# Kernel tuning notes

Hardware: AMD Instinct MI355X
Metric: run time of the kernel (lower is better)

The kernel has to match this reference:

```python
import jax, jax.numpy as jnp
import numpy as np

N = 50000        # nodes
E = 800000       # edges (avg degree 16)
D_IN = 128
HID = 128
K = 3


def cheb_edge_weights(row, col, n):
    # PyG ChebConv sym normalization with assumed lambda_max = 2.0:
    # L_hat = (2/lambda_max) * (I - D^-1/2 A D^-1/2) - I = -D^-1/2 A D^-1/2 (zero diagonal)
    mask = (row != col).astype(jnp.float32)  # remove_self_loops
    deg = jax.ops.segment_sum(mask, row, num_segments=n)
    dinv = jnp.where(deg > 0.0, jax.lax.rsqrt(jnp.maximum(deg, 1.0)), 0.0)
    return -dinv[row] * dinv[col] * mask  # [E]


def cheb_conv(x, row, col, w_edge, W, b, n):
    # Chebyshev recursion: Tx0=x, Tx1=L_hat x, Tx_k = 2 L_hat Tx_{k-1} - Tx_{k-2}
    def prop(h):  # sparse L_hat @ h via gather + segment_sum
        return jax.ops.segment_sum(w_edge[:, None] * h[col], row, num_segments=n)

    Tx0 = x
    out = Tx0 @ W[0]
    Tx1 = prop(Tx0)
    out = out + Tx1 @ W[1]
    for k in range(2, W.shape[0]):
        Tx2 = 2.0 * prop(Tx1) - Tx0
        out = out + Tx2 @ W[k]
        Tx0, Tx1 = Tx1, Tx2
    return out + b


def setup_inputs() -> dict:
    key = jax.random.key(0)
    ks = jax.random.split(key, 8)
    x = jax.random.normal(ks[0], (N, D_IN), dtype=jnp.float32)
    ei = jax.random.randint(ks[1], (2, E), 0, N, dtype=jnp.int32)
    s = 0.05
    W1 = jax.random.normal(ks[2], (K, D_IN, HID), dtype=jnp.float32) * s
    b1 = jnp.zeros((HID,), dtype=jnp.float32)
    W2 = jax.random.normal(ks[3], (K, HID, HID), dtype=jnp.float32) * s
    b2 = jnp.zeros((HID,), dtype=jnp.float32)
    W3 = jax.random.normal(ks[4], (K, HID, HID), dtype=jnp.float32) * s
    b3 = jnp.zeros((HID,), dtype=jnp.float32)
    return {"x": x, "ei": ei, "W1": W1, "b1": b1, "W2": W2, "b2": b2, "W3": W3, "b3": b3}


def reference(x, ei, W1, b1, W2, b2, W3, b3):
    row, col = ei[0], ei[1]
    w_edge = cheb_edge_weights(row, col, N)
    # layer chain: ChebConv -> ReLU -> dropout (eval mode: identity)
    h = jax.nn.relu(cheb_conv(x, row, col, w_edge, W1, b1, N))
    h = jax.nn.relu(cheb_conv(h, row, col, w_edge, W2, b2, N))
    h = jax.nn.relu(cheb_conv(h, row, col, w_edge, W3, b3, N))
    return h
```

## Files before the change

kernel.cpp:

```cpp
#include <hip/hip_runtime.h>
#include <hip/hip_bf16.h>

#define DFEAT 128

typedef _Float16 h2 __attribute__((ext_vector_type(2)));
typedef _Float16 f16x8 __attribute__((ext_vector_type(8)));
typedef float f32x4  __attribute__((ext_vector_type(4)));
typedef unsigned short u16x8 __attribute__((ext_vector_type(8)));

__device__ __forceinline__ unsigned short f16b(float f) {
    _Float16 hf = (_Float16)f;
    unsigned short b; __builtin_memcpy(&b, &hf, 2);
    return b;
}
__device__ __forceinline__ unsigned pack_f16(float lo, float hi) {
    return (unsigned)f16b(lo) | ((unsigned)f16b(hi) << 16);
}
__device__ __forceinline__ float h2f(h2 v) { float f; __builtin_memcpy(&f, &v, 4); return f; }
__device__ __forceinline__ h2 f2h(float f) { h2 v; __builtin_memcpy(&v, &f, 4); return v; }


__global__ void conv_kernel(const float2* __restrict__ x, unsigned* __restrict__ xb, int npk,
                            const float* __restrict__ W1, const float* __restrict__ W2,
                            const float* __restrict__ W3, unsigned short* __restrict__ Wt,
                            int* __restrict__ deg8, int N) {
    int id = blockIdx.x * blockDim.x + threadIdx.x;
    int gstride = gridDim.x * blockDim.x;
    for (int i = id; i < 8 * N; i += gstride) deg8[i] = 0;
    if (id < npk) {
        float2 v = x[id];
        xb[id] = pack_f16(v.x, v.y);
        return;
    }
    int id2 = id - npk;
    const int PER = 3 * DFEAT * DFEAT;
    if (id2 < 3 * PER) {
        int layer = id2 / PER;
        int rem = id2 - layer * PER;
        const float* W = (layer == 0) ? W1 : ((layer == 1) ? W2 : W3);
        int seg = rem >> 14;
        int k   = (rem >> 7) & 127;
        int nn  = rem & 127;
        float w = W[rem];
        if (seg == 0) w -= W[rem + 2 * DFEAT * DFEAT];
        else if (seg == 2) w *= 2.f;
        Wt[layer * PER + (seg << 14) + (nn << 7) + k] = f16b(w);
    }
}

__global__ void deg_kernel(const int* __restrict__ ei, int* __restrict__ deg8, int E, int N) {
    int e = blockIdx.x * blockDim.x + threadIdx.x;
    if (e < E) {
        int r = ei[e];
        int c = ei[E + e];
        if (r != c) atomicAdd(&deg8[(blockIdx.x & 7) * N + r], 1);
    }
}

__global__ __launch_bounds__(1024) void scan1_kernel(const int* __restrict__ deg8,
                                                     int* __restrict__ poff,
                                                     int* __restrict__ row_ptr,
                                                     int* __restrict__ bsum,
                                                     float* __restrict__ dinv, int n) {
    __shared__ int wsums[16];
    int t = threadIdx.x;
    int idx = blockIdx.x * 1024 + t;
    int tot = 0;
    if (idx < n) {
        int run = 0;
        #pragma unroll
        for (int p = 0; p < 8; ++p) {
            int d = deg8[p * n + idx];
            poff[p * n + idx] = run;
            run += d;
        }
        tot = run;
        dinv[idx] = (tot > 0) ? rsqrtf((float)tot) : 0.f;
    }
    int vi = tot;
    #pragma unroll
    for (int off = 1; off < 64; off <<= 1) {
        int x = __shfl_up(vi, off);
        if ((t & 63) >= off) vi += x;
    }
    if ((t & 63) == 63) wsums[t >> 6] = vi;
    __syncthreads();
    if (t < 16) {
        int s = wsums[t];
        int si = s;
        #pragma unroll
        for (int off = 1; off < 16; off <<= 1) {
            int x = __shfl_up(si, off);
            if (t >= off) si += x;
        }
        wsums[t] = si - s;
        if (t == 15) bsum[blockIdx.x] = si;
    }
    __syncthreads();
    if (idx < n) row_ptr[idx + 1] = wsums[t >> 6] + vi;
}

__global__ __launch_bounds__(1024) void scan3_kernel(int* __restrict__ row_ptr,
                                                     const int* __restrict__ bsum, int n) {
    __shared__ int soff;
    int t = threadIdx.x;
    if (t < 64) {
        int v = 0;
        for (int k = t; k < (int)blockIdx.x; k += 64) v += bsum[k];
        #pragma unroll
        for (int off = 32; off > 0; off >>= 1) v += __shfl_down(v, off);
        if (t == 0) soff = v;
    }
    __syncthreads();
    int idx = blockIdx.x * 1024 + t;
    if (idx == 0) row_ptr[0] = 0;
    if (idx < n) row_ptr[idx + 1] += soff;
}

__global__ void fill_kernel(const int* __restrict__ ei, const int* __restrict__ row_ptr,
                            int* __restrict__ poff, const float* __restrict__ dinv,
                            unsigned* __restrict__ e_cw, int E, int N) {
    int e = blockIdx.x * blockDim.x + threadIdx.x;
    if (e < E) {
        int r = ei[e];
        int c = ei[E + e];
        if (r != c) {
            int p = blockIdx.x & 7;
            int k = atomicAdd(&poff[p * N + r], 1);
            int pos = row_ptr[r] + k;
            float w = -dinv[r] * dinv[c];
            e_cw[pos] = (unsigned)c | ((unsigned)f16b(w) << 16);
        }
    }
}

__global__ __launch_bounds__(256) void prop_f16_kernel(
    const uint2* __restrict__ hin2, uint2* __restrict__ hout2,
    const int* __restrict__ row_ptr, const unsigned* __restrict__ e_cw, int n)
{
    int wv = __builtin_amdgcn_readfirstlane(threadIdx.x >> 6);
    int node = blockIdx.x * 4 + wv;
    if (node >= n) return;
    const int lane = threadIdx.x & 63;
    const int h = lane >> 5;
    const int s = lane & 31;
    int rs = row_ptr[node];
    int re = row_ptr[node + 1];

    h2 a01 = {(_Float16)0.f, (_Float16)0.f};
    h2 a23 = {(_Float16)0.f, (_Float16)0.f};

    for (int j = rs; j < re; j += 24) {
        uint2 vv[12]; unsigned ww[12];
        #pragma unroll
        for (int u = 0; u < 12; ++u) {
            int i0 = j + 2 * u;
            unsigned cw0 = (i0     < re) ? e_cw[i0]     : 0u;
            unsigned cw1 = (i0 + 1 < re) ? e_cw[i0 + 1] : 0u;
            unsigned cw = h ? cw1 : cw0;
            ww[u] = (cw & 0xffff0000u) | (cw >> 16);
            vv[u] = hin2[(size_t)(cw & 0xffffu) * 32 + s];
        }
        #pragma unroll
        for (int u = 0; u < 12; ++u) {
            h2 wp = f2h(__uint_as_float(ww[u]));
            a01 = f2h(__uint_as_float(vv[u].x)) * wp + a01;
            a23 = f2h(__uint_as_float(vv[u].y)) * wp + a23;
        }
    }
    a01 = a01 + f2h(__shfl_xor(h2f(a01), 32));
    a23 = a23 + f2h(__shfl_xor(h2f(a23), 32));

    if (h == 0) {
        uint2 o;
        o.x = __float_as_uint(h2f(a01));
        o.y = __float_as_uint(h2f(a23));
        hout2[(size_t)node * 32 + s] = o;
    }
}

#define WPAD 136
__global__ __launch_bounds__(256) void gemm3_mfma_kernel(
    const unsigned short* __restrict__ X0, const unsigned short* __restrict__ X1,
    const unsigned short* __restrict__ X2,
    const unsigned short* __restrict__ Wt, const float* __restrict__ bias,
    void* __restrict__ out, int n, int out_f16)
{
    __shared__ unsigned short Ws[DFEAT * WPAD];
    const int t    = threadIdx.x;
    const int wave = t >> 6;
    const int lane = t & 63;
    const int quad = lane >> 4;
    const int l16  = lane & 15;

    const int row_base = blockIdx.x * 128 + wave * 32;
    int r0 = row_base + l16;       if (r0 >= n) r0 = n - 1;
    int r1 = row_base + 16 + l16;  if (r1 >= n) r1 = n - 1;

    const unsigned short* Xps[3] = {X0, X1, X2};

    f32x4 acc[2][8];
    #pragma unroll
    for (int tt = 0; tt < 2; ++tt)
        #pragma unroll
        for (int c = 0; c < 8; ++c) acc[tt][c] = (f32x4){0.f, 0.f, 0.f, 0.f};

    const int srow = t >> 1;
    const int shalf = (t & 1) * 64;

    #pragma unroll
    for (int seg = 0; seg < 3; ++seg) {
        __syncthreads();
        const unsigned short* Wp = Wt + (seg << 14);
        #pragma unroll
        for (int i = 0; i < 8; ++i) {
            *(u16x8*)&Ws[srow * WPAD + shalf + i * 8] =
                *(const u16x8*)&Wp[srow * DFEAT + shalf + i * 8];
        }
        __syncthreads();
        const unsigned short* A0 = Xps[seg] + (size_t)r0 * DFEAT;
        const unsigned short* A1 = Xps[seg] + (size_t)r1 * DFEAT;
        #pragma unroll
        for (int kk = 0; kk < 4; ++kk) {
            const int ko = kk * 32 + quad * 8;
            f16x8 a0 = *(const f16x8*)(A0 + ko);
            f16x8 a1 = *(const f16x8*)(A1 + ko);
            #pragma unroll
            for (int c = 0; c < 8; ++c) {
                f16x8 b = *(const f16x8*)&Ws[(c * 16 + l16) * WPAD + ko];
                acc[0][c] = __builtin_amdgcn_mfma_f32_16x16x32_f16(a0, b, acc[0][c], 0, 0, 0);
                acc[1][c] = __builtin_amdgcn_mfma_f32_16x16x32_f16(a1, b, acc[1][c], 0, 0, 0);
            }
        }
    }

    #pragma unroll
    for (int tt = 0; tt < 2; ++tt) {
        int orow0 = blockIdx.x * 128 + wave * 32 + tt * 16 + quad * 4;
        #pragma unroll
        for (int c = 0; c < 8; ++c) {
            int col = c * 16 + l16;
            float bv = bias[col];
            #pragma unroll
            for (int r = 0; r < 4; ++r) {
                int orow = orow0 + r;
                if (orow < n) {
                    float v = fmaxf(acc[tt][c][r] + bv, 0.f);
                    if (out_f16)
                        ((unsigned short*)out)[(size_t)orow * DFEAT + col] = f16b(v);
                    else
                        ((float*)out)[(size_t)orow * DFEAT + col] = v;
                }
            }
        }
    }
}

extern "C" void kernel_launch(void* const* d_in, const int* in_sizes, int n_in,
                              void* d_out, int out_size, void* d_ws, size_t ws_size,
                              hipStream_t stream) {
    const float* x  = (const float*)d_in[0];
    const int*   ei = (const int*)d_in[1];
    const float* W1 = (const float*)d_in[2];
    const float* b1 = (const float*)d_in[3];
    const float* W2 = (const float*)d_in[4];
    const float* b2 = (const float*)d_in[5];
    const float* W3 = (const float*)d_in[6];
    const float* b3 = (const float*)d_in[7];

    const int N = in_sizes[0] / DFEAT;
    const int E = in_sizes[1] / 2;
    const int NPK = N * (DFEAT / 2);
    const int NB = (N + 1023) / 1024;

    unsigned* xb  = (unsigned*)d_ws;
    unsigned* t1b = xb  + NPK;
    unsigned* t2b = t1b + NPK;
    unsigned* ab  = t2b + NPK;
    unsigned short* wt = (unsigned short*)(ab + NPK);
    int*   deg8    = (int*)(wt + 3 * 3 * DFEAT * DFEAT);
    int*   poff    = deg8 + 8 * N;
    int*   row_ptr = poff + 8 * N;
    float* dinv    = (float*)(row_ptr + (N + 2));
    unsigned* e_cw = (unsigned*)(dinv + N);
    int*   bsum    = (int*)(e_cw + E);

    const int WELEM = 3 * DFEAT * DFEAT;
    const int CONVT = NPK + 3 * WELEM;
    conv_kernel<<<(CONVT + 255) / 256, 256, 0, stream>>>(
        (const float2*)x, xb, NPK, W1, W2, W3, wt, deg8, N);
    deg_kernel<<<(E + 255) / 256, 256, 0, stream>>>(ei, deg8, E, N);
    scan1_kernel<<<NB, 1024, 0, stream>>>(deg8, poff, row_ptr, bsum, dinv, N);
    scan3_kernel<<<NB, 1024, 0, stream>>>(row_ptr, bsum, N);
    fill_kernel<<<(E + 255) / 256, 256, 0, stream>>>(ei, row_ptr, poff, dinv, e_cw, E, N);

    const float* bl[3] = {b1, b2, b3};
    const unsigned* hin = xb;
    const int prop_grid = (N + 3) / 4;
    const int gemm_grid = (N + 127) / 128;
    for (int l = 0; l < 3; ++l) {
        prop_f16_kernel<<<prop_grid, 256, 0, stream>>>(
            (const uint2*)hin, (uint2*)t1b, row_ptr, e_cw, N);
        prop_f16_kernel<<<prop_grid, 256, 0, stream>>>(
            (const uint2*)t1b, (uint2*)t2b, row_ptr, e_cw, N);
        void* hout = (l == 2) ? d_out : (void*)ab;
        gemm3_mfma_kernel<<<gemm_grid, 256, 0, stream>>>(
            (const unsigned short*)hin, (const unsigned short*)t1b, (const unsigned short*)t2b,
            wt + l * WELEM, bl[l], hout, N, (l == 2) ? 0 : 1);
        hin = ab;
    }
}
```

Baseline: 388.4 us.

## Slice f16 feature matrices into four 32-column planes for cache-local gather

All f16 feature buffers are stored as four column slices of 32 features each (64 bytes per node per slice). The propagation kernel gains a slice grid dimension, so each wave gathers one slice, with 8 lanes per edge and 8 edges per step. The per-slice gather working set (N×64B, about 3.2MB) is meant to fit in cache and raise gather hit rates. The GEMM reads and writes the same sliced layout, and propagation outputs use nontemporal stores. In exchange the edge list and row pointers are read four times, each wave reduces across 8 edge groups with shuffles, and each edge fetches only 8 bytes per lane.

After: 582.9 us. +50.1%, slower.

```diff
diff --git a/kernel.cpp b/kernel.cpp
--- a/kernel.cpp
+++ b/kernel.cpp
@@ -7,6 +7,7 @@
 typedef _Float16 f16x8 __attribute__((ext_vector_type(8)));
 typedef float f32x4  __attribute__((ext_vector_type(4)));
 typedef unsigned short u16x8 __attribute__((ext_vector_type(8)));
+typedef unsigned u32x2 __attribute__((ext_vector_type(2)));
 
 __device__ __forceinline__ unsigned short f16b(float f) {
     _Float16 hf = (_Float16)f;
@@ -29,7 +30,9 @@
     for (int i = id; i < 8 * N; i += gstride) deg8[i] = 0;
     if (id < npk) {
         float2 v = x[id];
-        xb[id] = pack_f16(v.x, v.y);
+        int node = id >> 6;
+        int p    = id & 63;
+        xb[(size_t)(p >> 4) * (N * 16) + node * 16 + (p & 15)] = pack_f16(v.x, v.y);
         return;
     }
     int id2 = id - npk;
@@ -135,47 +138,52 @@
 }
 
 __global__ __launch_bounds__(256) void prop_f16_kernel(
-    const uint2* __restrict__ hin2, uint2* __restrict__ hout2,
-    const int* __restrict__ row_ptr, const unsigned* __restrict__ e_cw, int n)
+    const uint2* __restrict__ hin2, unsigned* __restrict__ hout,
+    const int* __restrict__ row_ptr, const unsigned* __restrict__ e_cw,
+    int n, int nbs)
 {
     int wv = __builtin_amdgcn_readfirstlane(threadIdx.x >> 6);
-    int node = blockIdx.x * 4 + wv;
+    int sl = blockIdx.x / nbs;
+    int node = (blockIdx.x - sl * nbs) * 4 + wv;
     if (node >= n) return;
     const int lane = threadIdx.x & 63;
-    const int h = lane >> 5;
-    const int s = lane & 31;
+    const int e = lane >> 3;
+    const int s = lane & 7;
     int rs = row_ptr[node];
     int re = row_ptr[node + 1];
+    const uint2* __restrict__ hsl = hin2 + (size_t)sl * n * 8;
 
     h2 a01 = {(_Float16)0.f, (_Float16)0.f};
     h2 a23 = {(_Float16)0.f, (_Float16)0.f};
 
     for (int j = rs; j < re; j += 24) {
-        uint2 vv[12]; unsigned ww[12];
-        #pragma unroll
-        for (int u = 0; u < 12; ++u) {
-            int i0 = j + 2 * u;
-            unsigned cw0 = (i0     < re) ? e_cw[i0]     : 0u;
-            unsigned cw1 = (i0 + 1 < re) ? e_cw[i0 + 1] : 0u;
-            unsigned cw = h ? cw1 : cw0;
+        uint2 vv[3]; unsigned ww[3];
+        #pragma unroll
+        for (int u = 0; u < 3; ++u) {
+            int i0 = j + u * 8 + e;
+            unsigned cw = (i0 < re) ? e_cw[i0] : 0u;
             ww[u] = (cw & 0xffff0000u) | (cw >> 16);
-            vv[u] = hin2[(size_t)(cw & 0xffffu) * 32 + s];
-        }
-        #pragma unroll
-        for (int u = 0; u < 12; ++u) {
+            vv[u] = hsl[(size_t)(cw & 0xffffu) * 8 + s];
+        }
+        #pragma unroll
+        for (int u = 0; u < 3; ++u) {
             h2 wp = f2h(__uint_as_float(ww[u]));
             a01 = f2h(__uint_as_float(vv[u].x)) * wp + a01;
             a23 = f2h(__uint_as_float(vv[u].y)) * wp + a23;
         }
     }
-    a01 = a01 + f2h(__shfl_xor(h2f(a01), 32));
-    a23 = a23 + f2h(__shfl_xor(h2f(a23), 32));
-
-    if (h == 0) {
-        uint2 o;
-        o.x = __float_as_uint(h2f(a01));
-        o.y = __float_as_uint(h2f(a23));
-        hout2[(size_t)node * 32 + s] = o;
+    #pragma unroll
+    for (int off = 8; off < 64; off <<= 1) {
+        a01 = a01 + f2h(__shfl_xor(h2f(a01), off));
+        a23 = a23 + f2h(__shfl_xor(h2f(a23), off));
+    }
+
+    if (lane < 8) {
+        u32x2 o;
+        o[0] = __float_as_uint(h2f(a01));
+        o[1] = __float_as_uint(h2f(a23));
+        u32x2* dst = (u32x2*)(hout + (((size_t)sl * n + node) * 8 + s) * 2);
+        __builtin_nontemporal_store(o, dst);
     }
 }
 
@@ -218,13 +226,13 @@
                 *(const u16x8*)&Wp[srow * DFEAT + shalf + i * 8];
         }
         __syncthreads();
-        const unsigned short* A0 = Xps[seg] + (size_t)r0 * DFEAT;
-        const unsigned short* A1 = Xps[seg] + (size_t)r1 * DFEAT;
+        const unsigned short* Ab = Xps[seg];
         #pragma unroll
         for (int kk = 0; kk < 4; ++kk) {
+            const size_t sbase = (size_t)kk * n * 32 + (size_t)quad * 8;
+            f16x8 a0 = *(const f16x8*)(Ab + sbase + (size_t)r0 * 32);
+            f16x8 a1 = *(const f16x8*)(Ab + sbase + (size_t)r1 * 32);
             const int ko = kk * 32 + quad * 8;
-            f16x8 a0 = *(const f16x8*)(A0 + ko);
-            f16x8 a1 = *(const f16x8*)(A1 + ko);
             #pragma unroll
             for (int c = 0; c < 8; ++c) {
                 f16x8 b = *(const f16x8*)&Ws[(c * 16 + l16) * WPAD + ko];
@@ -246,10 +254,12 @@
                 int orow = orow0 + r;
                 if (orow < n) {
                     float v = fmaxf(acc[tt][c][r] + bv, 0.f);
-                    if (out_f16)
-                        ((unsigned short*)out)[(size_t)orow * DFEAT + col] = f16b(v);
-                    else
+                    if (out_f16) {
+                        ((unsigned short*)out)[(size_t)(c >> 1) * n * 32 +
+                                               (size_t)orow * 32 + (c & 1) * 16 + l16] = f16b(v);
+                    } else {
                         ((float*)out)[(size_t)orow * DFEAT + col] = v;
+                    }
                 }
             }
         }
@@ -296,13 +306,14 @@
 
     const float* bl[3] = {b1, b2, b3};
     const unsigned* hin = xb;
-    const int prop_grid = (N + 3) / 4;
+    const int nbs = (N + 3) / 4;
+    const int prop_grid = 4 * nbs;
     const int gemm_grid = (N + 127) / 128;
     for (int l = 0; l < 3; ++l) {
         prop_f16_kernel<<<prop_grid, 256, 0, stream>>>(
-            (const uint2*)hin, (uint2*)t1b, row_ptr, e_cw, N);
+            (const uint2*)hin, t1b, row_ptr, e_cw, N, nbs);
         prop_f16_kernel<<<prop_grid, 256, 0, stream>>>(
-            (const uint2*)t1b, (uint2*)t2b, row_ptr, e_cw, N);
+            (const uint2*)t1b, t2b, row_ptr, e_cw, N, nbs);
         void* hout = (l == 2) ? d_out : (void*)ab;
         gemm3_mfma_kernel<<<gemm_grid, 256, 0, stream>>>(
             (const unsigned short*)hin, (const unsigned short*)t1b, (const unsigned short*)t2b,
```
